# Kernel optimization log

Measured on AMD Instinct MI355X. Metric: run time of the kernel, lower is better.

## Reference

```python
import jax, jax.numpy as jnp
import numpy as np

E = 1024   # embed_dim
H = 16     # num_heads
D = E // H # head_dim
T, N, M, B = 1024, 1024, 1023, 4  # tgt len, leaves, tree nodes, batch


def setup_inputs() -> dict:
    key0 = jax.random.key(0)
    ks = jax.random.split(key0, 8)
    s = 1.0 / np.sqrt(E).astype(np.float32)  # xavier-ish scale
    return {
        "query": jax.random.normal(ks[0], (T, B, E), jnp.float32),
        "key": jax.random.normal(ks[1], (N, B, E), jnp.float32),
        "node_key": jax.random.normal(ks[2], (M, B, E), jnp.float32),
        "in_proj_weight": jax.random.normal(ks[3], (3 * E, E), jnp.float32) * s,
        "in_proj_bias": jnp.zeros((3 * E,), jnp.float32),
        "out_w": jax.random.normal(ks[4], (E, E), jnp.float32) * s,
        "out_b": jnp.zeros((E,), jnp.float32),
        "dw_w": jax.random.normal(ks[5], (H, E), jnp.float32) * s,
        "dw_b": jnp.zeros((H,), jnp.float32),
        "key_padding_mask": jnp.zeros((B, N), bool),
        "node_padding_mask": jnp.zeros((B, M), bool),
    }


def reference(query, key, node_key, in_proj_weight, in_proj_bias,
              out_w, out_b, dw_w, dw_b, key_padding_mask, node_padding_mask):
    t, b, e = query.shape
    n, m = key.shape[0], node_key.shape[0]
    d = e // H
    scaling = d ** -0.5
    # fused in-proj slices (F.linear: y = x W^T + bias)
    Wq, Wk, Wv = in_proj_weight[:e], in_proj_weight[e:2 * e], in_proj_weight[2 * e:]
    bq, bk, bv = in_proj_bias[:e], in_proj_bias[e:2 * e], in_proj_bias[2 * e:]
    q = (query @ Wq.T + bq) * scaling
    k = key @ Wk.T + bk
    v = key @ Wv.T + bv
    nk = node_key @ Wk.T + bk          # node_kv_same: nodes share kv projection
    nv = node_key @ Wv.T + bv

    def heads(x, L):  # [L,B,E] -> [B,H,L,D]
        return x.reshape(L, b, H, d).transpose(1, 2, 0, 3)

    qh, kh, vh = heads(q, t), heads(k, n), heads(v, n)
    nkh, nvh = heads(nk, m), heads(nv, m)

    # per-head affinity weights for merged stack nodes (dwstack, sigmoid act)
    dw = jax.nn.sigmoid(node_key @ dw_w.T + dw_b)   # [M,B,H]
    nvh = nvh * dw.transpose(1, 2, 0)[..., None]    # weighted node values

    s_leaf = jnp.einsum('bhtd,bhnd->bhtn', qh, kh)
    s_node = jnp.einsum('bhtd,bhmd->bhtm', qh, nkh)
    neg = jnp.finfo(s_leaf.dtype).min
    s_leaf = jnp.where(key_padding_mask[:, None, None, :], neg, s_leaf)
    s_node = jnp.where(node_padding_mask[:, None, None, :], neg, s_node)

    attn = jax.nn.softmax(jnp.concatenate([s_leaf, s_node], axis=-1), axis=-1)
    vals = jnp.concatenate([vh, nvh], axis=2)       # [B,H,N+M,D]
    o = jnp.einsum('bhts,bhsd->bhtd', attn, vals)   # [B,H,T,D]
    o = o.transpose(2, 0, 1, 3).reshape(t, b, e)
    return o @ out_w.T + out_b
```

## Files before the change

### kernel.cpp

```cpp
#include <hip/hip_runtime.h>
#include <cstdint>
#include <cstddef>

using short8 = __attribute__((ext_vector_type(8))) short;
using f32x4  = __attribute__((ext_vector_type(4))) float;

constexpr int T_ = 1024;
constexpr int N_ = 1024;
constexpr int M_ = 1023;
constexpr int B_ = 4;
constexpr int E_ = 1024;
constexpr int H_ = 16;
constexpr int D_ = 64;

#define MFMA16(a, b, c) __builtin_amdgcn_mfma_f32_16x16x32_bf16((a), (b), (c), 0, 0, 0)

__device__ __forceinline__ unsigned short f2bf(float f) {
    unsigned int u = __float_as_uint(f);
    u += 0x7FFF + ((u >> 16) & 1);
    return (unsigned short)(u >> 16);
}
__device__ __forceinline__ float bf2f(unsigned short s) {
    return __uint_as_float(((unsigned int)s) << 16);
}

__device__ __forceinline__ unsigned int cvt_pk_bf16(float lo, float hi) {
    unsigned int r;
    asm("v_cvt_pk_bf16_f32 %0, %1, %2" : "=v"(r) : "v"(lo), "v"(hi));
    return r;
}

typedef __attribute__((address_space(1))) const unsigned char gc_byte;
typedef __attribute__((address_space(3))) unsigned char lds_byte;
__device__ __forceinline__ void gload16(const void* g, void* lds) {
    __builtin_amdgcn_global_load_lds((gc_byte*)(uintptr_t)g,
                                     (lds_byte*)(unsigned int)(uintptr_t)lds,
                                     16, 0, 0);
}

__global__ void f2bf_kernel(const float* __restrict__ src,
                            unsigned short* __restrict__ dst, int n, int npad)
{
    int i = (blockIdx.x * 256 + threadIdx.x) * 4;
    if (i >= npad) return;
    if (i + 4 <= n) {
        const float4 v = *reinterpret_cast<const float4*>(src + i);
        ushort4 o;
        o.x = f2bf(v.x); o.y = f2bf(v.y); o.z = f2bf(v.z); o.w = f2bf(v.w);
        *reinterpret_cast<ushort4*>(dst + i) = o;
    } else {
        for (int k = 0; k < 4; ++k)
            dst[i + k] = (i + k < n) ? f2bf(src[i + k]) : (unsigned short)0;
    }
}

__global__ void f2bf_hilo_kernel(const float* __restrict__ src,
                                 unsigned short* __restrict__ dhi,
                                 unsigned short* __restrict__ dlo, int n)
{
    int i = (blockIdx.x * 256 + threadIdx.x) * 4;
    if (i >= n) return;
    const float4 v = *reinterpret_cast<const float4*>(src + i);
    float a[4] = {v.x, v.y, v.z, v.w};
    ushort4 hi, lo;
    unsigned short h[4], l[4];
    #pragma unroll
    for (int k = 0; k < 4; ++k) {
        h[k] = f2bf(a[k]);
        l[k] = f2bf(a[k] - bf2f(h[k]));
    }
    hi.x = h[0]; hi.y = h[1]; hi.z = h[2]; hi.w = h[3];
    lo.x = l[0]; lo.y = l[1]; lo.z = l[2]; lo.w = l[3];
    *reinterpret_cast<ushort4*>(dhi + i) = hi;
    *reinterpret_cast<ushort4*>(dlo + i) = lo;
}

__global__ void dw_kernel(const float* __restrict__ node_key,
                          const float* __restrict__ dw_w,
                          const float* __restrict__ dw_b,
                          float* __restrict__ dwb)
{
    __shared__ float rowbuf[E_];
    const int r = blockIdx.x;
    const int tid = threadIdx.x;
    for (int idx = tid; idx < E_; idx += 256)
        rowbuf[idx] = node_key[(size_t)r * E_ + idx];
    __syncthreads();
    const int h = tid >> 4;
    const int lane = tid & 15;
    float acc = 0.f;
    const float* wrow = dw_w + (size_t)h * E_;
    for (int k = lane; k < E_; k += 16)
        acc = fmaf(rowbuf[k], wrow[k], acc);
    acc += __shfl_xor(acc, 8);
    acc += __shfl_xor(acc, 4);
    acc += __shfl_xor(acc, 2);
    acc += __shfl_xor(acc, 1);
    if (lane == 0) {
        float x = acc + dw_b[h];
        dwb[(size_t)r * H_ + h] = 1.f / (1.f + __expf(-x));
    }
}

__global__ __launch_bounds__(256) void proj_mfma(
    const unsigned short* __restrict__ xq,
    const unsigned short* __restrict__ xk,
    const unsigned short* __restrict__ xn,
    const unsigned short* __restrict__ wbf,
    const float* __restrict__ ipb,
    const float* __restrict__ dwb,
    unsigned short* __restrict__ qb,
    unsigned short* __restrict__ kb,
    unsigned short* __restrict__ vtb,
    unsigned short* __restrict__ nkb,
    unsigned short* __restrict__ nvtb)
{
    __shared__ unsigned short LDS[3][2][128 * 32];

    const unsigned short* A;
    const unsigned short* W;
    const float* bias;
    const float* dwm = nullptr;
    unsigned short* out;
    int epi;
    float scale = 1.f;
    switch (blockIdx.z) {
      case 0:  A = xq; W = wbf;           bias = ipb;        out = qb;   epi = 1; scale = 0.18033688011112042f; break;
      case 1:  A = xk; W = wbf + 1048576; bias = ipb + 1024; out = kb;   epi = 1; break;
      case 2:  A = xk; W = wbf + 2097152; bias = ipb + 2048; out = vtb;  epi = 2; break;
      case 3:  A = xn; W = wbf + 1048576; bias = ipb + 1024; out = nkb;  epi = 1; break;
      default: A = xn; W = wbf + 2097152; bias = ipb + 2048; out = nvtb; epi = 2; dwm = dwb; break;
    }

    const int tid = threadIdx.x;
    const int l = tid & 63, w = tid >> 6;
    const int brow = blockIdx.y * 128;
    const int bcol = blockIdx.x * 128;

    const int ch0 = w * 64 + l;
    const int ch1 = 256 + w * 64 + l;
    const unsigned short* gA0 = A + (size_t)(brow + (ch0 >> 2)) * E_ + (ch0 & 3) * 8;
    const unsigned short* gA1 = A + (size_t)(brow + (ch1 >> 2)) * E_ + (ch1 & 3) * 8;
    const unsigned short* gW0 = W + (size_t)(bcol + (ch0 >> 2)) * E_ + (ch0 & 3) * 8;
    const unsigned short* gW1 = W + (size_t)(bcol + (ch1 >> 2)) * E_ + (ch1 & 3) * 8;

    auto STAGE = [&](int buf, int kt) {
        gload16(gA0 + kt, &LDS[buf][0][(size_t)w * 512]);
        gload16(gA1 + kt, &LDS[buf][0][(size_t)(4 + w) * 512]);
        gload16(gW0 + kt, &LDS[buf][1][(size_t)w * 512]);
        gload16(gW1 + kt, &LDS[buf][1][(size_t)(4 + w) * 512]);
    };

    f32x4 acc[4][4];
    #pragma unroll
    for (int m = 0; m < 4; ++m)
        #pragma unroll
        for (int n = 0; n < 4; ++n)
            acc[m][n] = (f32x4){0.f, 0.f, 0.f, 0.f};

    const int wr = (w >> 1) * 64, wc = (w & 1) * 64;
    const int fr = l & 15, ko = (l >> 4) * 8;

    STAGE(0, 0);
    STAGE(1, 32);

    for (int t = 0; t < 32; ++t) {
        if (t < 31) asm volatile("s_waitcnt vmcnt(4)" ::: "memory");
        else        asm volatile("s_waitcnt vmcnt(0)" ::: "memory");
        __builtin_amdgcn_sched_barrier(0);
        __builtin_amdgcn_s_barrier();
        __builtin_amdgcn_sched_barrier(0);

        if (t < 30) STAGE((t + 2) % 3, (t + 2) * 32);

        const int cur = t % 3;
        short8 av[4], bv[4];
        #pragma unroll
        for (int m = 0; m < 4; ++m)
            av[m] = *reinterpret_cast<const short8*>(&LDS[cur][0][(wr + m * 16 + fr) * 32 + ko]);
        #pragma unroll
        for (int n = 0; n < 4; ++n)
            bv[n] = *reinterpret_cast<const short8*>(&LDS[cur][1][(wc + n * 16 + fr) * 32 + ko]);
        __builtin_amdgcn_s_setprio(1);
        #pragma unroll
        for (int m = 0; m < 4; ++m)
            #pragma unroll
            for (int n = 0; n < 4; ++n)
                acc[m][n] = MFMA16(av[m], bv[n], acc[m][n]);
        __builtin_amdgcn_s_setprio(0);
    }

    #pragma unroll
    for (int n = 0; n < 4; ++n) {
        const int c = bcol + wc + n * 16 + fr;
        const float bi = bias[c];
        #pragma unroll
        for (int m = 0; m < 4; ++m) {
            #pragma unroll
            for (int j = 0; j < 4; ++j) {
                const int r = brow + wr + m * 16 + (l >> 4) * 4 + j;
                float v = (acc[m][n][j] + bi) * scale;
                const int rn = r >> 2, b = r & 3, hh = c >> 6, dd = c & 63;
                if (epi == 1) {
                    out[((size_t)(b * H_ + hh) * 1024 + rn) * 64 + dd] = f2bf(v);
                } else {
                    if (dwm) v *= dwm[(size_t)r * H_ + hh];
                    out[(((size_t)(b * H_ + hh) * 32 + (rn >> 5)) * 64 + dd) * 32 + (rn & 31)] = f2bf(v);
                }
            }
        }
    }
}

__global__ __launch_bounds__(256) void outproj_mfma(
    const unsigned short* __restrict__ ahi,
    const unsigned short* __restrict__ alo,
    const unsigned short* __restrict__ whi,
    const unsigned short* __restrict__ wlo,
    const float* __restrict__ out_b,
    float* __restrict__ out)
{
    __shared__ unsigned short LDS[2][4][128 * 32];

    const int tid = threadIdx.x;
    const int l = tid & 63, w = tid >> 6;
    const int brow = blockIdx.y * 128;
    const int bcol = blockIdx.x * 128;

    const int ch0 = w * 64 + l;
    const int ch1 = 256 + w * 64 + l;
    const size_t ra0 = (size_t)(brow + (ch0 >> 2)) * E_ + (ch0 & 3) * 8;
    const size_t ra1 = (size_t)(brow + (ch1 >> 2)) * E_ + (ch1 & 3) * 8;
    const size_t rb0 = (size_t)(bcol + (ch0 >> 2)) * E_ + (ch0 & 3) * 8;
    const size_t rb1 = (size_t)(bcol + (ch1 >> 2)) * E_ + (ch1 & 3) * 8;

    auto STAGE = [&](int buf, int kt) {
        gload16(ahi + ra0 + kt, &LDS[buf][0][(size_t)w * 512]);
        gload16(ahi + ra1 + kt, &LDS[buf][0][(size_t)(4 + w) * 512]);
        gload16(alo + ra0 + kt, &LDS[buf][1][(size_t)w * 512]);
        gload16(alo + ra1 + kt, &LDS[buf][1][(size_t)(4 + w) * 512]);
        gload16(whi + rb0 + kt, &LDS[buf][2][(size_t)w * 512]);
        gload16(whi + rb1 + kt, &LDS[buf][2][(size_t)(4 + w) * 512]);
        gload16(wlo + rb0 + kt, &LDS[buf][3][(size_t)w * 512]);
        gload16(wlo + rb1 + kt, &LDS[buf][3][(size_t)(4 + w) * 512]);
    };

    f32x4 acc[4][4];
    #pragma unroll
    for (int m = 0; m < 4; ++m)
        #pragma unroll
        for (int n = 0; n < 4; ++n)
            acc[m][n] = (f32x4){0.f, 0.f, 0.f, 0.f};

    const int wr = (w >> 1) * 64, wc = (w & 1) * 64;
    const int fr = l & 15, ko = (l >> 4) * 8;

    STAGE(0, 0);
    __syncthreads();
    for (int t = 0; t < 32; ++t) {
        const int cur = t & 1;
        if (t < 31) STAGE(cur ^ 1, (t + 1) * 32);
        short8 ah[4], al[4], bh[4], bl[4];
        #pragma unroll
        for (int m = 0; m < 4; ++m) {
            ah[m] = *reinterpret_cast<const short8*>(&LDS[cur][0][(wr + m * 16 + fr) * 32 + ko]);
            al[m] = *reinterpret_cast<const short8*>(&LDS[cur][1][(wr + m * 16 + fr) * 32 + ko]);
        }
        #pragma unroll
        for (int n = 0; n < 4; ++n) {
            bh[n] = *reinterpret_cast<const short8*>(&LDS[cur][2][(wc + n * 16 + fr) * 32 + ko]);
            bl[n] = *reinterpret_cast<const short8*>(&LDS[cur][3][(wc + n * 16 + fr) * 32 + ko]);
        }
        #pragma unroll
        for (int m = 0; m < 4; ++m)
            #pragma unroll
            for (int n = 0; n < 4; ++n) {
                acc[m][n] = MFMA16(ah[m], bh[n], acc[m][n]);
                acc[m][n] = MFMA16(al[m], bh[n], acc[m][n]);
                acc[m][n] = MFMA16(ah[m], bl[n], acc[m][n]);
            }
        if (t < 31) __syncthreads();
    }

    #pragma unroll
    for (int n = 0; n < 4; ++n) {
        const int c = bcol + wc + n * 16 + fr;
        const float bi = out_b[c];
        #pragma unroll
        for (int m = 0; m < 4; ++m)
            #pragma unroll
            for (int j = 0; j < 4; ++j) {
                const int r = brow + wr + m * 16 + (l >> 4) * 4 + j;
                out[(size_t)r * E_ + c] = acc[m][n][j] + bi;
            }
    }
}

__global__ __launch_bounds__(256) void attn_mfma(
    const unsigned short* __restrict__ qbf,
    const unsigned short* __restrict__ kbf,
    const unsigned short* __restrict__ nkbf,
    const unsigned short* __restrict__ vtb,
    const unsigned short* __restrict__ nvtb,
    const unsigned char* __restrict__ kpm,
    const unsigned char* __restrict__ npm,
    float* __restrict__ pacc,
    float* __restrict__ pm,
    float* __restrict__ pl)
{
    __shared__ unsigned short Kl[2][64 * 64];
    __shared__ unsigned short Vl[2][64 * 64];
    __shared__ float maskF[1024];
    __shared__ int tmask[16];

    const int tid = threadIdx.x;
    const int l = tid & 63, w = tid >> 6;
    const int bh = blockIdx.x, b = bh >> 4;
    const int t0 = blockIdx.y * 64;
    const int half = blockIdx.z;

    const unsigned short* kb_ = half ? nkbf : kbf;
    const unsigned short* vb_ = half ? nvtb : vtb;

    if (tid < 16) tmask[tid] = 0;
    __syncthreads();
    for (int s = tid; s < 1024; s += 256) {
        int masked;
        if (half == 0) masked = kpm[(size_t)b * N_ + s] ? 1 : 0;
        else           masked = (s < M_ && !npm[(size_t)b * M_ + s]) ? 0 : 1;
        maskF[s] = masked ? -60000.f : 0.f;
        if (masked) atomicOr(&tmask[s >> 6], 1);
    }

    auto STAGE = [&](int buf, int s0) {
        #pragma unroll
        for (int u = 0; u < 2; ++u) {
            const int c = u * 256 + tid;
            const int krow = c >> 3;
            const int kcol = ((c & 7) * 16) ^ ((krow & 7) << 4);
            gload16((const unsigned char*)kb_ +
                        ((size_t)(bh * 1024 + s0 + krow) * 64) * 2 + kcol,
                    (unsigned char*)&Kl[buf][0] + c * 16);
            const int kg = c >> 6;
            const int dd = c & 63;
            const int kv = s0 + kg * 8;
            const int kp = kv >> 5;
            gload16((const unsigned char*)vb_ +
                        (((size_t)(bh * 32 + kp) * 64 + dd) * 32 + (kv & 31)) * 2,
                    (unsigned char*)&Vl[buf][0] + c * 16);
        }
    };

    const int g = l >> 4;
    const int q = l & 15;

    const int qrow = t0 + w * 16 + q;
    const short8 aq0 = *reinterpret_cast<const short8*>(&qbf[((size_t)bh * T_ + qrow) * 64 + g * 8]);
    const short8 aq1 = *reinterpret_cast<const short8*>(&qbf[((size_t)bh * T_ + qrow) * 64 + 32 + g * 8]);

    float mold = -30000.f, lr = 0.f;
    f32x4 acco[4];
    #pragma unroll
    for (int n = 0; n < 4; ++n) acco[n] = (f32x4){0.f, 0.f, 0.f, 0.f};

    const int ksw = (l & 7) << 4;
    const int kb0 = q * 128 + ((g * 16) ^ ksw);
    const int kb1 = q * 128 + ((64 + g * 16) ^ ksw);
    const int vb0 = g * 1024 + q * 16;

    const int src0 = (g & 1) * 32 + q;
    const int src1 = src0 + 16;
    const bool selhi = (l & 32) != 0;

    STAGE(0, 0);
    __syncthreads();

    for (int it = 0; it < 16; ++it) {
        const int s0 = it * 64;
        const int cur = it & 1;
        if (it < 15) STAGE(cur ^ 1, s0 + 64);

        const unsigned char* const Kc = (const unsigned char*)&Kl[cur][0];
        const unsigned char* const Vc = (const unsigned char*)&Vl[cur][0];

        f32x4 accs[4];
        #pragma unroll
        for (int n = 0; n < 4; ++n) accs[n] = (f32x4){0.f, 0.f, 0.f, 0.f};
        __builtin_amdgcn_s_setprio(1);
        #pragma unroll
        for (int n = 0; n < 4; ++n) {
            const short8 k0 = *reinterpret_cast<const short8*>(Kc + n * 2048 + kb0);
            const short8 k1 = *reinterpret_cast<const short8*>(Kc + n * 2048 + kb1);
            accs[n] = MFMA16(k0, aq0, accs[n]);
            accs[n] = MFMA16(k1, aq1, accs[n]);
        }
        __builtin_amdgcn_s_setprio(0);

        if (tmask[s0 >> 6]) {
            #pragma unroll
            for (int n = 0; n < 4; ++n) {
                const float4 mz = *reinterpret_cast<const float4*>(&maskF[s0 + n * 16 + g * 4]);
                accs[n][0] += mz.x;
                accs[n][1] += mz.y;
                accs[n][2] += mz.z;
                accs[n][3] += mz.w;
            }
        }

        float mx = -60000.f;
        #pragma unroll
        for (int n = 0; n < 4; ++n)
            #pragma unroll
            for (int j = 0; j < 4; ++j) mx = fmaxf(mx, accs[n][j]);
        mx = fmaxf(mx, __shfl_xor(mx, 16));
        mx = fmaxf(mx, __shfl_xor(mx, 32));

        if (__any(mx > mold + 8.f)) {
            const float mn = fmaxf(mold, mx);
            const float f = __builtin_amdgcn_exp2f(mold - mn);
            mold = mn;
            lr *= f;
            #pragma unroll
            for (int n = 0; n < 4; ++n)
                #pragma unroll
                for (int j = 0; j < 4; ++j) acco[n][j] *= f;
        }

        float p[4][4];
        float ps = 0.f;
        #pragma unroll
        for (int n = 0; n < 4; ++n)
            #pragma unroll
            for (int j = 0; j < 4; ++j) {
                p[n][j] = __builtin_amdgcn_exp2f(accs[n][j] - mold);
                ps += p[n][j];
            }
        ps += __shfl_xor(ps, 16);
        ps += __shfl_xor(ps, 32);
        lr += ps;

        unsigned int ppk[4][2];
        #pragma unroll
        for (int n = 0; n < 4; ++n) {
            ppk[n][0] = cvt_pk_bf16(p[n][0], p[n][1]);
            ppk[n][1] = cvt_pk_bf16(p[n][2], p[n][3]);
        }

        union UF { int4 i4; short8 s8; } pf[2];
        #pragma unroll
        for (int h = 0; h < 2; ++h) {
            const unsigned int a0 = __shfl((int)ppk[2 * h][0],     src0);
            const unsigned int b0 = __shfl((int)ppk[2 * h + 1][0], src0);
            const unsigned int a1 = __shfl((int)ppk[2 * h][1],     src0);
            const unsigned int b1 = __shfl((int)ppk[2 * h + 1][1], src0);
            const unsigned int a2 = __shfl((int)ppk[2 * h][0],     src1);
            const unsigned int b2 = __shfl((int)ppk[2 * h + 1][0], src1);
            const unsigned int a3 = __shfl((int)ppk[2 * h][1],     src1);
            const unsigned int b3 = __shfl((int)ppk[2 * h + 1][1], src1);
            pf[h].i4.x = selhi ? b0 : a0;
            pf[h].i4.y = selhi ? b1 : a1;
            pf[h].i4.z = selhi ? b2 : a2;
            pf[h].i4.w = selhi ? b3 : a3;
        }

        __builtin_amdgcn_s_setprio(1);
        #pragma unroll
        for (int n = 0; n < 4; ++n) {
            const short8 v0 = *reinterpret_cast<const short8*>(Vc + n * 256 + vb0);
            const short8 v1 = *reinterpret_cast<const short8*>(Vc + 4096 + n * 256 + vb0);
            acco[n] = MFMA16(v0, pf[0].s8, acco[n]);
            acco[n] = MFMA16(v1, pf[1].s8, acco[n]);
        }
        __builtin_amdgcn_s_setprio(0);

        __syncthreads();
    }

    const size_t row = ((size_t)(half * 64 + bh)) * 1024 + t0 + w * 16 + q;
    #pragma unroll
    for (int n = 0; n < 4; ++n) {
        float4 st;
        st.x = acco[n][0];
        st.y = acco[n][1];
        st.z = acco[n][2];
        st.w = acco[n][3];
        *reinterpret_cast<float4*>(&pacc[row * 64 + n * 16 + g * 4]) = st;
    }
    if (l < 16) {
        pm[row] = mold;
        pl[row] = lr;
    }
}

__global__ void merge_kernel(const float* __restrict__ pacc,
                             const float* __restrict__ pm,
                             const float* __restrict__ pl,
                             unsigned short* __restrict__ ohi,
                             unsigned short* __restrict__ olo)
{
    const int g = blockIdx.x * 256 + threadIdx.x;
    const int row = g >> 4;
    const int d4 = (g & 15) * 4;
    const int bh = row >> 10, t = row & 1023;
    const int b = bh >> 4, h = bh & 15;

    const float m0 = pm[row], m1 = pm[65536 + row];
    const float l0 = pl[row], l1 = pl[65536 + row];
    const float ms = fmaxf(m0, m1);
    const float w0 = __builtin_amdgcn_exp2f(m0 - ms);
    const float w1 = __builtin_amdgcn_exp2f(m1 - ms);
    const float den = 1.f / (l0 * w0 + l1 * w1);

    const float4 a0 = *reinterpret_cast<const float4*>(&pacc[(size_t)row * 64 + d4]);
    const float4 a1 = *reinterpret_cast<const float4*>(&pacc[(size_t)(65536 + row) * 64 + d4]);

    float o[4] = {
        (a0.x * w0 + a1.x * w1) * den,
        (a0.y * w0 + a1.y * w1) * den,
        (a0.z * w0 + a1.z * w1) * den,
        (a0.w * w0 + a1.w * w1) * den,
    };
    ushort4 vh_, vl_;
    unsigned short hh[4], ll[4];
    #pragma unroll
    for (int k = 0; k < 4; ++k) {
        hh[k] = f2bf(o[k]);
        ll[k] = f2bf(o[k] - bf2f(hh[k]));
    }
    vh_.x = hh[0]; vh_.y = hh[1]; vh_.z = hh[2]; vh_.w = hh[3];
    vl_.x = ll[0]; vl_.y = ll[1]; vl_.z = ll[2]; vl_.w = ll[3];
    const size_t oidx = ((size_t)t * B_ + b) * E_ + h * D_ + d4;
    *reinterpret_cast<ushort4*>(&ohi[oidx]) = vh_;
    *reinterpret_cast<ushort4*>(&olo[oidx]) = vl_;
}

extern "C" void kernel_launch(void* const* d_in, const int* in_sizes, int n_in,
                              void* d_out, int out_size, void* d_ws, size_t ws_size,
                              hipStream_t stream) {
    const float* query    = (const float*)d_in[0];
    const float* key      = (const float*)d_in[1];
    const float* node_key = (const float*)d_in[2];
    const float* ipw      = (const float*)d_in[3];
    const float* ipb      = (const float*)d_in[4];
    const float* out_w    = (const float*)d_in[5];
    const float* out_b    = (const float*)d_in[6];
    const float* dw_w     = (const float*)d_in[7];
    const float* dw_b     = (const float*)d_in[8];
    const unsigned char* kpm = (const unsigned char*)d_in[9];
    const unsigned char* npm = (const unsigned char*)d_in[10];
    float* out = (float*)d_out;

    char* p = (char*)d_ws;
    auto alloc = [&](size_t bytes) {
        char* r = p;
        p += (bytes + 255) & ~(size_t)255;
        return r;
    };
    unsigned short* xq    = (unsigned short*)alloc((size_t)4096 * 1024 * 2);
    unsigned short* xk    = (unsigned short*)alloc((size_t)4096 * 1024 * 2);
    unsigned short* xn    = (unsigned short*)alloc((size_t)4096 * 1024 * 2);
    unsigned short* wbf   = (unsigned short*)alloc((size_t)3072 * 1024 * 2);
    (void)alloc((size_t)2 * 1024 * 1024);
    unsigned short* wohi  = (unsigned short*)alloc((size_t)1024 * 1024 * 2);
    unsigned short* wolo  = (unsigned short*)alloc((size_t)1024 * 1024 * 2);
    unsigned short* qb    = (unsigned short*)alloc((size_t)64 * 1024 * 64 * 2);
    unsigned short* kb_   = (unsigned short*)alloc((size_t)64 * 1024 * 64 * 2);
    unsigned short* nkb   = (unsigned short*)alloc((size_t)64 * 1024 * 64 * 2);
    unsigned short* vtb   = (unsigned short*)alloc((size_t)64 * 1024 * 64 * 2);
    unsigned short* nvtb  = (unsigned short*)alloc((size_t)64 * 1024 * 64 * 2);
    unsigned short* ohi   = (unsigned short*)alloc((size_t)4096 * 1024 * 2);
    unsigned short* olo   = (unsigned short*)alloc((size_t)4096 * 1024 * 2);
    float*          dwb   = (float*)alloc((size_t)4096 * 16 * 4);
    float*          pm    = (float*)alloc((size_t)2 * 65536 * 4);
    float*          pl    = (float*)alloc((size_t)2 * 65536 * 4);
    float*          pacc  = (float*)xq;

    const dim3 blk(256);

    f2bf_kernel<<<dim3(4096), blk, 0, stream>>>(query,    xq, 4194304, 4194304);
    f2bf_kernel<<<dim3(4096), blk, 0, stream>>>(key,      xk, 4194304, 4194304);
    f2bf_kernel<<<dim3(4096), blk, 0, stream>>>(node_key, xn, 4190208, 4194304);
    f2bf_kernel<<<dim3(3072), blk, 0, stream>>>(ipw,      wbf, 3145728, 3145728);
    f2bf_hilo_kernel<<<dim3(1024), blk, 0, stream>>>(out_w, wohi, wolo, 1048576);

    dw_kernel<<<dim3(M_ * B_), blk, 0, stream>>>(node_key, dw_w, dw_b, dwb);

    proj_mfma<<<dim3(8, 32, 5), blk, 0, stream>>>(xq, xk, xn, wbf, ipb, dwb,
                                                  qb, kb_, vtb, nkb, nvtb);

    attn_mfma<<<dim3(64, 16, 2), blk, 0, stream>>>(qb, kb_, nkb, vtb, nvtb,
                                                   kpm, npm, pacc, pm, pl);

    merge_kernel<<<dim3(4096), blk, 0, stream>>>(pacc, pm, pl, ohi, olo);

    outproj_mfma<<<dim3(8, 32), blk, 0, stream>>>(ohi, olo, wohi, wolo, out_b, out);
}
```

Before: 256.8 us.

## Merge fp32-to-bf16 conversions into one launch and XOR-swizzle GEMM LDS tiles

Replaces five separate conversion launches (query, key, node_key, in-proj weight, out-proj hi/lo split) with one kernel that dispatches on block index, removing launch overhead and tail gaps between them. It also applies an XOR swizzle to the 16-byte chunk positions in both the projection and output-projection GEMMs. The global-load source columns are permuted to match the permuted LDS read offsets, which is meant to cut LDS bank conflicts on the fragment reads. The swizzle must match exactly between the global_load_lds writes and the fragment reads, or results are silently wrong.

```diff
diff --git a/kernel.cpp b/kernel.cpp
--- a/kernel.cpp
+++ b/kernel.cpp
@@ -38,11 +38,10 @@
                                      16, 0, 0);
 }
 
-__global__ void f2bf_kernel(const float* __restrict__ src,
-                            unsigned short* __restrict__ dst, int n, int npad)
+__device__ __forceinline__ void conv_body(const float* __restrict__ src,
+                                          unsigned short* __restrict__ dst,
+                                          int i, int n)
 {
-    int i = (blockIdx.x * 256 + threadIdx.x) * 4;
-    if (i >= npad) return;
     if (i + 4 <= n) {
         const float4 v = *reinterpret_cast<const float4*>(src + i);
         ushort4 o;
@@ -54,25 +53,44 @@
     }
 }
 
-__global__ void f2bf_hilo_kernel(const float* __restrict__ src,
-                                 unsigned short* __restrict__ dhi,
-                                 unsigned short* __restrict__ dlo, int n)
+__global__ void conv_all(const float* __restrict__ query,
+                         const float* __restrict__ key,
+                         const float* __restrict__ node_key,
+                         const float* __restrict__ ipw,
+                         const float* __restrict__ out_w,
+                         unsigned short* __restrict__ xq,
+                         unsigned short* __restrict__ xk,
+                         unsigned short* __restrict__ xn,
+                         unsigned short* __restrict__ wbf,
+                         unsigned short* __restrict__ wohi,
+                         unsigned short* __restrict__ wolo)
 {
-    int i = (blockIdx.x * 256 + threadIdx.x) * 4;
-    if (i >= n) return;
-    const float4 v = *reinterpret_cast<const float4*>(src + i);
-    float a[4] = {v.x, v.y, v.z, v.w};
-    ushort4 hi, lo;
-    unsigned short h[4], l[4];
-    #pragma unroll
-    for (int k = 0; k < 4; ++k) {
-        h[k] = f2bf(a[k]);
-        l[k] = f2bf(a[k] - bf2f(h[k]));
-    }
-    hi.x = h[0]; hi.y = h[1]; hi.z = h[2]; hi.w = h[3];
-    lo.x = l[0]; lo.y = l[1]; lo.z = l[2]; lo.w = l[3];
-    *reinterpret_cast<ushort4*>(dhi + i) = hi;
-    *reinterpret_cast<ushort4*>(dlo + i) = lo;
+    const int blk = blockIdx.x;
+    const int tid = threadIdx.x;
+    if (blk < 4096) {
+        conv_body(query, xq, (blk * 256 + tid) * 4, 4194304);
+    } else if (blk < 8192) {
+        conv_body(key, xk, ((blk - 4096) * 256 + tid) * 4, 4194304);
+    } else if (blk < 12288) {
+        conv_body(node_key, xn, ((blk - 8192) * 256 + tid) * 4, 4190208);
+    } else if (blk < 15360) {
+        conv_body(ipw, wbf, ((blk - 12288) * 256 + tid) * 4, 3145728);
+    } else {
+        const int i = ((blk - 15360) * 256 + tid) * 4;
+        const float4 v = *reinterpret_cast<const float4*>(out_w + i);
+        float a[4] = {v.x, v.y, v.z, v.w};
+        ushort4 hi, lo;
+        unsigned short h[4], l[4];
+        #pragma unroll
+        for (int k = 0; k < 4; ++k) {
+            h[k] = f2bf(a[k]);
+            l[k] = f2bf(a[k] - bf2f(h[k]));
+        }
+        hi.x = h[0]; hi.y = h[1]; hi.z = h[2]; hi.w = h[3];
+        lo.x = l[0]; lo.y = l[1]; lo.z = l[2]; lo.w = l[3];
+        *reinterpret_cast<ushort4*>(wohi + i) = hi;
+        *reinterpret_cast<ushort4*>(wolo + i) = lo;
+    }
 }
 
 __global__ void dw_kernel(const float* __restrict__ node_key,
@@ -139,10 +157,12 @@
 
     const int ch0 = w * 64 + l;
     const int ch1 = 256 + w * 64 + l;
-    const unsigned short* gA0 = A + (size_t)(brow + (ch0 >> 2)) * E_ + (ch0 & 3) * 8;
-    const unsigned short* gA1 = A + (size_t)(brow + (ch1 >> 2)) * E_ + (ch1 & 3) * 8;
-    const unsigned short* gW0 = W + (size_t)(bcol + (ch0 >> 2)) * E_ + (ch0 & 3) * 8;
-    const unsigned short* gW1 = W + (size_t)(bcol + (ch1 >> 2)) * E_ + (ch1 & 3) * 8;
+    const int u0 = ((ch0 & 3) ^ ((ch0 >> 3) & 3)) * 8;
+    const int u1 = ((ch1 & 3) ^ ((ch1 >> 3) & 3)) * 8;
+    const unsigned short* gA0 = A + (size_t)(brow + (ch0 >> 2)) * E_ + u0;
+    const unsigned short* gA1 = A + (size_t)(brow + (ch1 >> 2)) * E_ + u1;
+    const unsigned short* gW0 = W + (size_t)(bcol + (ch0 >> 2)) * E_ + u0;
+    const unsigned short* gW1 = W + (size_t)(bcol + (ch1 >> 2)) * E_ + u1;
 
     auto STAGE = [&](int buf, int kt) {
         gload16(gA0 + kt, &LDS[buf][0][(size_t)w * 512]);
@@ -159,7 +179,8 @@
             acc[m][n] = (f32x4){0.f, 0.f, 0.f, 0.f};
 
     const int wr = (w >> 1) * 64, wc = (w & 1) * 64;
-    const int fr = l & 15, ko = (l >> 4) * 8;
+    const int fr = l & 15;
+    const int ko = (((l >> 4) ^ ((fr >> 1) & 3))) * 8;
 
     STAGE(0, 0);
     STAGE(1, 32);
@@ -229,10 +250,12 @@
 
     const int ch0 = w * 64 + l;
     const int ch1 = 256 + w * 64 + l;
-    const size_t ra0 = (size_t)(brow + (ch0 >> 2)) * E_ + (ch0 & 3) * 8;
-    const size_t ra1 = (size_t)(brow + (ch1 >> 2)) * E_ + (ch1 & 3) * 8;
-    const size_t rb0 = (size_t)(bcol + (ch0 >> 2)) * E_ + (ch0 & 3) * 8;
-    const size_t rb1 = (size_t)(bcol + (ch1 >> 2)) * E_ + (ch1 & 3) * 8;
+    const int u0 = ((ch0 & 3) ^ ((ch0 >> 3) & 3)) * 8;
+    const int u1 = ((ch1 & 3) ^ ((ch1 >> 3) & 3)) * 8;
+    const size_t ra0 = (size_t)(brow + (ch0 >> 2)) * E_ + u0;
+    const size_t ra1 = (size_t)(brow + (ch1 >> 2)) * E_ + u1;
+    const size_t rb0 = (size_t)(bcol + (ch0 >> 2)) * E_ + u0;
+    const size_t rb1 = (size_t)(bcol + (ch1 >> 2)) * E_ + u1;
 
     auto STAGE = [&](int buf, int kt) {
         gload16(ahi + ra0 + kt, &LDS[buf][0][(size_t)w * 512]);
@@ -253,7 +276,8 @@
             acc[m][n] = (f32x4){0.f, 0.f, 0.f, 0.f};
 
     const int wr = (w >> 1) * 64, wc = (w & 1) * 64;
-    const int fr = l & 15, ko = (l >> 4) * 8;
+    const int fr = l & 15;
+    const int ko = (((l >> 4) ^ ((fr >> 1) & 3))) * 8;
 
     STAGE(0, 0);
     __syncthreads();
@@ -577,11 +601,8 @@
 
     const dim3 blk(256);
 
-    f2bf_kernel<<<dim3(4096), blk, 0, stream>>>(query,    xq, 4194304, 4194304);
-    f2bf_kernel<<<dim3(4096), blk, 0, stream>>>(key,      xk, 4194304, 4194304);
-    f2bf_kernel<<<dim3(4096), blk, 0, stream>>>(node_key, xn, 4190208, 4194304);
-    f2bf_kernel<<<dim3(3072), blk, 0, stream>>>(ipw,      wbf, 3145728, 3145728);
-    f2bf_hilo_kernel<<<dim3(1024), blk, 0, stream>>>(out_w, wohi, wolo, 1048576);
+    conv_all<<<dim3(16384), blk, 0, stream>>>(query, key, node_key, ipw, out_w,
+                                              xq, xk, xn, wbf, wohi, wolo);
 
     dw_kernel<<<dim3(M_ * B_), blk, 0, stream>>>(node_key, dw_w, dw_b, dwb);
 
```

After: 254.0 us. About the same (-1.1%).
